# Kernel optimization log

Hardware: AMD Instinct MI355X
Metric: run time of the kernel (lower is better)

## Reference

```python
import jax, jax.numpy as jnp
import numpy as np

NUM_GROUPS = 8
EPS = 1e-5


def setup_inputs() -> dict:
    key = jax.random.key(0)
    ks = jax.random.split(key, 3)
    B, C, H, W = 32, 256, 64, 64
    x = jax.random.normal(ks[0], (B, C, H, W), dtype=jnp.float32)
    gn_weight = jnp.ones((C,), dtype=jnp.float32)
    gn_bias = jnp.zeros((C,), dtype=jnp.float32)
    # 1x1 convs stored as [out_ch, in_ch] matrices (kernel dims squeezed)
    qkv_weight = jax.random.normal(ks[1], (3 * C, C), dtype=jnp.float32) * (1.0 / np.sqrt(C))
    qkv_bias = jnp.zeros((3 * C,), dtype=jnp.float32)
    proj_weight = jax.random.normal(ks[2], (C, C), dtype=jnp.float32) * (1.0 / np.sqrt(C))
    proj_bias = jnp.zeros((C,), dtype=jnp.float32)
    return {
        "x": x,
        "gn_weight": gn_weight,
        "gn_bias": gn_bias,
        "qkv_weight": qkv_weight,
        "qkv_bias": qkv_bias,
        "proj_weight": proj_weight,
        "proj_bias": proj_bias,
    }


def _group_norm(x, weight, bias):
    B, C, H, W = x.shape
    g = x.reshape(B, NUM_GROUPS, C // NUM_GROUPS, H, W)
    mean = g.mean(axis=(2, 3, 4), keepdims=True)
    var = g.var(axis=(2, 3, 4), keepdims=True)
    g = (g - mean) * jax.lax.rsqrt(var + EPS)
    x = g.reshape(B, C, H, W)
    return x * weight[None, :, None, None] + bias[None, :, None, None]


def reference(x, gn_weight, gn_bias, qkv_weight, qkv_bias, proj_weight, proj_bias):
    B, C, H, W = x.shape
    x_norm = _group_norm(x, gn_weight, gn_bias)
    # 1x1 conv C -> 3C: contraction over channel dim
    qkv = jnp.einsum('bchw,oc->bohw', x_norm, qkv_weight) + qkv_bias[None, :, None, None]
    qkv = qkv.reshape(B, 3, C, H * W)  # [B,3,C,HW]
    q, k, v = qkv[:, 0], qkv[:, 1], qkv[:, 2]  # each [B,C,HW]
    # channel attention: attn is [B,C,C], softmax over last (key-channel) dim
    scale = 1.0 / jnp.sqrt(jnp.asarray(C, dtype=x.dtype))
    scores = jnp.einsum('bcn,bdn->bcd', q, k) * scale
    attn = jax.nn.softmax(scores, axis=-1)
    out = jnp.einsum('bcd,bdn->bcn', attn, v).reshape(B, C, H, W)
    proj = jnp.einsum('bchw,oc->bohw', out, proj_weight) + proj_bias[None, :, None, None]
    return x + proj
```

## Files before the change

### kernel.cpp

```cpp
#include <hip/hip_runtime.h>


#define B_ 32
#define C_ 256
#define N_ 4096
#define GSIZE (32 * N_)
#define EPSV 1e-5f
#define SCALE 0.0625f

#define OFF_SC    0
#define OFF_SH    8192
#define OFF_RS    16384
#define OFF_RSP   24576
#define OFF_SQP   90112
#define OFF_RALL  155648
#define OFF_CV    180224
#define OFF_CONST 188416
#define OFF_WVT   196608
#define OFF_GM    229376
#define OFF_AT    2326528
#define OFF_S16   4423680
#define OFF_GP    5472256

typedef _Float16 half_t;
typedef half_t f16x8 __attribute__((ext_vector_type(8)));
typedef float f32x16 __attribute__((ext_vector_type(16)));

__global__ __launch_bounds__(512, 1) void gram_v4_k(const float* __restrict__ x,
                                                    float* __restrict__ ws) {
  __shared__ __align__(16) char hb[2][32768];
  int b = blockIdx.x >> 3, ks = blockIdx.x & 7;
  int t = threadIdx.x;
  const float* xb = x + (size_t)b * (C_ * (size_t)N_) + ks * 512;
  int lane = t & 63, w = t >> 6;
  int wm = w >> 2, wn = w & 3, r31 = lane & 31, hi = lane >> 5;
  int lrow = t >> 4, lc4 = t & 15;
  const float* lbase = xb + (size_t)lrow * N_ + lc4 * 4;
  f32x16 acc[4][2] = {};
  float4 stg[2][8];
  float rs[8] = {0.f, 0.f, 0.f, 0.f, 0.f, 0.f, 0.f, 0.f};
  float rq[8] = {0.f, 0.f, 0.f, 0.f, 0.f, 0.f, 0.f, 0.f};

#define LOADV(sb, c)                                                      \
  _Pragma("unroll") for (int p = 0; p < 8; ++p)                           \
      stg[sb][p] = *(const float4*)(lbase + (size_t)p * 32 * N_ + (c) * 64);

#define WRITEV(sb, buf)                                                   \
  {                                                                       \
    char* bp = hb[buf];                                                   \
    _Pragma("unroll") for (int p = 0; p < 8; ++p) {                       \
      float4 v = stg[sb][p];                                              \
      rs[p] += v.x + v.y + v.z + v.w;                                     \
      rq[p] += v.x * v.x + v.y * v.y + v.z * v.z + v.w * v.w;             \
      union { half_t h[4]; uint2 u; } H;                                  \
      H.h[0] = (half_t)v.x; H.h[1] = (half_t)v.y;                         \
      H.h[2] = (half_t)v.z; H.h[3] = (half_t)v.w;                         \
      int row = lrow + p * 32;                                            \
      int slot = (lc4 >> 1) ^ (row & 7);                                  \
      *(uint2*)(bp + row * 128 + slot * 16 + (lc4 & 1) * 8) = H.u;        \
    }                                                                     \
  }

  LOADV(0, 0);
  LOADV(1, 1);
  WRITEV(0, 0);
  __syncthreads();
  for (int c = 0; c < 8; ++c) {
    int buf = c & 1;
#pragma unroll
    for (int kk = 0; kk < 4; ++kk) {
      int kb = kk * 32 + hi * 16;
      f16x8 Af[4], Bf[2];
#pragma unroll
      for (int m = 0; m < 4; ++m) {
        int row = wm * 128 + m * 32 + r31;
        Af[m] = *(const f16x8*)(hb[buf] + row * 128 + (((kb >> 4) ^ (row & 7)) * 16));
      }
#pragma unroll
      for (int n = 0; n < 2; ++n) {
        int row = wn * 64 + n * 32 + r31;
        Bf[n] = *(const f16x8*)(hb[buf] + row * 128 + (((kb >> 4) ^ (row & 7)) * 16));
      }
#pragma unroll
      for (int m = 0; m < 4; ++m)
#pragma unroll
        for (int n = 0; n < 2; ++n)
          acc[m][n] = __builtin_amdgcn_mfma_f32_32x32x16_f16(Af[m], Bf[n], acc[m][n], 0, 0, 0);
    }
    if (c < 7) {
      int nb = (c + 1) & 1;
      WRITEV(nb, nb);
      if (c < 6) LOADV(buf, c + 2);
      __syncthreads();
    }
  }
#pragma unroll
  for (int p = 0; p < 8; ++p) {
    float s = rs[p], q = rq[p];
    s += __shfl_xor(s, 1); s += __shfl_xor(s, 2);
    s += __shfl_xor(s, 4); s += __shfl_xor(s, 8);
    q += __shfl_xor(q, 1); q += __shfl_xor(q, 2);
    q += __shfl_xor(q, 4); q += __shfl_xor(q, 8);
    if ((t & 15) == 0) {
      int row = lrow + p * 32;
      ws[OFF_RSP + (size_t)blockIdx.x * 256 + row] = s;
      ws[OFF_SQP + (size_t)blockIdx.x * 256 + row] = q;
    }
  }
  half_t* Gp = (half_t*)(ws + OFF_GP) + (size_t)blockIdx.x * 65536;
#pragma unroll
  for (int m = 0; m < 4; ++m)
#pragma unroll
    for (int n = 0; n < 2; ++n)
#pragma unroll
      for (int r = 0; r < 16; ++r) {
        int gr = wm * 128 + m * 32 + (r & 3) + 8 * (r >> 2) + 4 * hi;
        int gc = wn * 64 + n * 32 + r31;
        Gp[gr * 256 + gc] = (half_t)acc[m][n][r];
      }
#undef LOADV
#undef WRITEV
}

__global__ __launch_bounds__(256) void gsum_k(float* __restrict__ ws) {
  int bx = blockIdx.x;
  int b = bx >> 6, seg = bx & 63;
  int e0 = seg * 1024 + threadIdx.x * 4;
  const half_t* Gp = (const half_t*)(ws + OFF_GP) + (size_t)b * 8 * 65536 + e0;
  float4 s = {0.f, 0.f, 0.f, 0.f};
#pragma unroll
  for (int ks = 0; ks < 8; ++ks) {
    union { uint2 u; half_t h[4]; } P;
    P.u = *(const uint2*)(Gp + (size_t)ks * 65536);
    s.x += (float)P.h[0]; s.y += (float)P.h[1];
    s.z += (float)P.h[2]; s.w += (float)P.h[3];
  }
  *(float4*)(ws + OFF_GM + (size_t)b * 65536 + e0) = s;
}

__global__ __launch_bounds__(256) void prep_k(const float* __restrict__ gw,
                                              const float* __restrict__ gb,
                                              const float* __restrict__ qkvw,
                                              float* __restrict__ ws) {
  int b = blockIdx.x, t = threadIdx.x;
  __shared__ float sL[256], qL[256], svecs[256], gmean[8], grstd[8];
  float s = 0.f, q = 0.f;
#pragma unroll
  for (int ks = 0; ks < 8; ++ks) {
    s += ws[OFF_RSP + (b * 8 + ks) * 256 + t];
    q += ws[OFF_SQP + (b * 8 + ks) * 256 + t];
  }
  ws[OFF_RS + b * 256 + t] = s;
  sL[t] = s; qL[t] = q;
  __syncthreads();
  if (t < 8) {
    float gs = 0.f, gq = 0.f;
    for (int i = 0; i < 32; ++i) { gs += sL[t * 32 + i]; gq += qL[t * 32 + i]; }
    float mean = gs * (1.f / GSIZE);
    float var = gq * (1.f / GSIZE) - mean * mean;
    gmean[t] = mean;
    grstd[t] = rsqrtf(var + EPSV);
  }
  __syncthreads();
  int g = t >> 5;
  float sc = grstd[g] * gw[t];
  float sh = gb[t] - gmean[g] * sc;
  ws[OFF_SC + b * 256 + t] = sc;
  ws[OFF_SH + b * 256 + t] = sh;
  float sv = s * sc + 4096.f * sh;
  svecs[t] = sv;
  __syncthreads();
  for (int oo = 0; oo < 3; ++oo) {
    int o = t + oo * 256;
    const float* wr = qkvw + (size_t)o * 256;
    float acc = 0.f;
#pragma unroll 8
    for (int c = 0; c < 256; ++c) acc += wr[c] * svecs[c];
    ws[OFF_RALL + b * 768 + o] = acc;
  }
}

__global__ __launch_bounds__(256) void wvt_k(const float* __restrict__ qkvw,
                                             float* __restrict__ ws) {
  int e = blockIdx.x, d = threadIdx.x;
  float v = qkvw[(size_t)(512 + d) * 256 + e];
  ((half_t*)(ws + OFF_WVT))[e * 256 + d] = (half_t)v;
}

__global__ __launch_bounds__(256) void fused_logits_k(
    const float* __restrict__ qkvw, const float* __restrict__ qkvb,
    float* __restrict__ ws) {
  int b = blockIdx.y, r0 = blockIdx.x * 32;
  int t = threadIdx.x, lane = t & 63, w = t >> 6, r31 = lane & 31, hi = lane >> 5;
  __shared__ __align__(16) char GHL[32768];
  __shared__ __align__(16) char AHL[8192];
  __shared__ float T1s[32][257];
  __shared__ float scs[256], shs[256], rss[256];
  __shared__ float bk_s[256], rk_s[256], bq_s[32], rq_s[32];
  scs[t] = ws[OFF_SC + b * 256 + t];
  shs[t] = ws[OFF_SH + b * 256 + t];
  rss[t] = ws[OFF_RS + b * 256 + t];
  bk_s[t] = qkvb[256 + t];
  rk_s[t] = ws[OFF_RALL + b * 768 + 256 + t];
  if (t < 32) {
    bq_s[t] = qkvb[r0 + t];
    rq_s[t] = ws[OFF_RALL + b * 768 + r0 + t];
  }
  __syncthreads();
  const float* Graw = ws + OFF_GM + (size_t)b * 65536;
  f32x16 acc[2] = {};
  for (int k0 = 0; k0 < 256; k0 += 32) {
    {
      int row = t >> 3, c4 = t & 7;
      float4 v = *(const float4*)(qkvw + (size_t)(r0 + row) * 256 + k0 + c4 * 4);
      union { half_t h[4]; uint2 u; } H, L;
      float vv[4] = {v.x, v.y, v.z, v.w};
#pragma unroll
      for (int j = 0; j < 4; ++j) {
        half_t h = (half_t)vv[j];
        H.h[j] = h; L.h[j] = (half_t)(vv[j] - (float)h);
      }
      int s8 = row & 7;
      *(uint2*)(AHL + row * 128 + (((c4 >> 1) ^ s8) * 16) + (c4 & 1) * 8) = H.u;
      *(uint2*)(AHL + row * 128 + ((((c4 >> 1) + 4) ^ s8) * 16) + (c4 & 1) * 8) = L.u;
    }
    {
#pragma unroll
      for (int p = 0; p < 8; ++p) {
        int f = t + p * 256;
        int row = f >> 3, c4 = f & 7;
        float4 gv = *(const float4*)(Graw + (size_t)row * 256 + k0 + c4 * 4);
        float scd = scs[row], shd = shs[row], rsd = rss[row];
        union { half_t h[4]; uint2 u; } H, L;
        float gvv[4] = {gv.x, gv.y, gv.z, gv.w};
#pragma unroll
        for (int j = 0; j < 4; ++j) {
          int cc = k0 + c4 * 4 + j;
          float scc = scs[cc], shc = shs[cc];
          float val = scc * scd * gvv[j] + scc * shd * rss[cc] +
                      shc * scd * rsd + 4096.f * shc * shd;
          half_t h = (half_t)val;
          H.h[j] = h; L.h[j] = (half_t)(val - (float)h);
        }
        int s8 = row & 7;
        *(uint2*)(GHL + row * 128 + (((c4 >> 1) ^ s8) * 16) + (c4 & 1) * 8) = H.u;
        *(uint2*)(GHL + row * 128 + ((((c4 >> 1) + 4) ^ s8) * 16) + (c4 & 1) * 8) = L.u;
      }
    }
    __syncthreads();
#pragma unroll
    for (int kk = 0; kk < 2; ++kk) {
      int kb = kk * 32 + hi * 16;
      int arow = r31;
      f16x8 Aq = *(const f16x8*)(AHL + arow * 128 + (((kb >> 4) ^ (arow & 7)) * 16));
#pragma unroll
      for (int n = 0; n < 2; ++n) {
        int row = w * 64 + n * 32 + r31;
        int s8 = row & 7;
        f16x8 Bh = *(const f16x8*)(GHL + row * 128 + (((kb >> 4) ^ s8) * 16));
        f16x8 Bl = *(const f16x8*)(GHL + row * 128 + ((((kb >> 4) + 4) ^ s8) * 16));
        acc[n] = __builtin_amdgcn_mfma_f32_32x32x16_f16(Aq, Bh, acc[n], 0, 0, 0);
        acc[n] = __builtin_amdgcn_mfma_f32_32x32x16_f16(Aq, Bl, acc[n], 0, 0, 0);
      }
    }
    __syncthreads();
  }
#pragma unroll
  for (int n = 0; n < 2; ++n)
#pragma unroll
    for (int r = 0; r < 16; ++r)
      T1s[(r & 3) + 8 * (r >> 2) + 4 * hi][w * 64 + n * 32 + r31] = acc[n][r];
  __syncthreads();
  f32x16 acc2[2] = {};
  for (int k0 = 0; k0 < 256; k0 += 64) {
    {
      int row = t >> 3;
#pragma unroll
      for (int u = 0; u < 2; ++u) {
        int c4 = (t & 7) + u * 8;
        float vv[4];
#pragma unroll
        for (int j = 0; j < 4; ++j) vv[j] = T1s[row][k0 + c4 * 4 + j];
        union { half_t h[4]; uint2 u2; } H, L;
#pragma unroll
        for (int j = 0; j < 4; ++j) {
          half_t h = (half_t)vv[j];
          H.h[j] = h; L.h[j] = (half_t)(vv[j] - (float)h);
        }
        int s16 = row & 15;
        *(uint2*)(AHL + row * 256 + (((c4 >> 1) ^ s16) * 16) + (c4 & 1) * 8) = H.u2;
        *(uint2*)(AHL + row * 256 + ((((c4 >> 1) + 8) ^ s16) * 16) + (c4 & 1) * 8) = L.u2;
      }
    }
    {
#pragma unroll
      for (int p = 0; p < 16; ++p) {
        int f = t + p * 256;
        int row = f >> 4, c4 = f & 15;
        float4 v = *(const float4*)(qkvw + (size_t)(256 + row) * 256 + k0 + c4 * 4);
        union { half_t h[4]; uint2 u; } H;
        H.h[0] = (half_t)v.x; H.h[1] = (half_t)v.y;
        H.h[2] = (half_t)v.z; H.h[3] = (half_t)v.w;
        int slot = (c4 >> 1) ^ (row & 7);
        *(uint2*)(GHL + row * 128 + slot * 16 + (c4 & 1) * 8) = H.u;
      }
    }
    __syncthreads();
#pragma unroll
    for (int kk = 0; kk < 4; ++kk) {
      int kb = kk * 32 + hi * 16;
      int arow = r31;
      int s16 = arow & 15;
      f16x8 Ah = *(const f16x8*)(AHL + arow * 256 + (((kb >> 4) ^ s16) * 16));
      f16x8 Al = *(const f16x8*)(AHL + arow * 256 + ((((kb >> 4) + 8) ^ s16) * 16));
#pragma unroll
      for (int n = 0; n < 2; ++n) {
        int row = w * 64 + n * 32 + r31;
        f16x8 Bf = *(const f16x8*)(GHL + row * 128 + (((kb >> 4) ^ (row & 7)) * 16));
        acc2[n] = __builtin_amdgcn_mfma_f32_32x32x16_f16(Ah, Bf, acc2[n], 0, 0, 0);
        acc2[n] = __builtin_amdgcn_mfma_f32_32x32x16_f16(Al, Bf, acc2[n], 0, 0, 0);
      }
    }
    __syncthreads();
  }
#pragma unroll
  for (int n = 0; n < 2; ++n)
#pragma unroll
    for (int r = 0; r < 16; ++r) {
      int rr = (r & 3) + 8 * (r >> 2) + 4 * hi;
      int cc = w * 64 + n * 32 + r31;
      float v = acc2[n][r];
      v = (v + bq_s[rr] * rk_s[cc] + bk_s[cc] * rq_s[rr] +
           4096.f * bq_s[rr] * bk_s[cc]) * SCALE;
      T1s[rr][cc] = v;
    }
  __syncthreads();
  bk_s[t] = qkvb[512 + t];
  __syncthreads();
  {
    int row = t >> 3, ls = t & 7;
    float m = -1e30f;
#pragma unroll
    for (int i = 0; i < 32; ++i) m = fmaxf(m, T1s[row][ls + i * 8]);
    m = fmaxf(m, __shfl_xor(m, 1));
    m = fmaxf(m, __shfl_xor(m, 2));
    m = fmaxf(m, __shfl_xor(m, 4));
    float s = 0.f, cvp = 0.f;
#pragma unroll
    for (int i = 0; i < 32; ++i) {
      int col = ls + i * 8;
      float e = __expf(T1s[row][col] - m);
      T1s[row][col] = e;
      s += e;
      cvp += e * bk_s[col];
    }
    s += __shfl_xor(s, 1); s += __shfl_xor(s, 2); s += __shfl_xor(s, 4);
    cvp += __shfl_xor(cvp, 1); cvp += __shfl_xor(cvp, 2); cvp += __shfl_xor(cvp, 4);
    float inv = 1.f / s;
#pragma unroll
    for (int i = 0; i < 32; ++i) T1s[row][ls + i * 8] *= inv;
    if (ls == 0) ws[OFF_CV + b * 256 + r0 + row] = cvp * inv;
  }
  __syncthreads();
  {
    float* ATb = ws + OFF_AT + (size_t)b * 65536;
#pragma unroll
    for (int u = 0; u < 8; ++u) {
      float4 v = {T1s[u * 4 + 0][t], T1s[u * 4 + 1][t], T1s[u * 4 + 2][t],
                  T1s[u * 4 + 3][t]};
      *(float4*)(ATb + (size_t)t * 256 + r0 + u * 4) = v;
    }
  }
}

__global__ __launch_bounds__(256) void fused_s_k(const float* __restrict__ pw,
                                                 const float* __restrict__ pb,
                                                 float* __restrict__ ws) {
  int b = blockIdx.y, r0 = blockIdx.x * 32;
  int t = threadIdx.x, lane = t & 63, w = t >> 6, r31 = lane & 31, hi = lane >> 5;
  __shared__ __align__(16) char GHL[32768];
  __shared__ __align__(16) char AHL[8192];
  __shared__ float T1s[32][257];
  __shared__ float cvs[256];
  cvs[t] = ws[OFF_CV + b * 256 + t];
  __syncthreads();
  const float* ATb = ws + OFF_AT + (size_t)b * 65536;
  f32x16 acc[2] = {};
  for (int k0 = 0; k0 < 256; k0 += 64) {
    {
#pragma unroll
      for (int p = 0; p < 2; ++p) {
        int f = t + p * 256;
        int row = f >> 4, c4 = f & 15;
        float4 v = *(const float4*)(pw + (size_t)(r0 + row) * 256 + k0 + c4 * 4);
        union { half_t h[4]; uint2 u; } H;
        H.h[0] = (half_t)v.x; H.h[1] = (half_t)v.y;
        H.h[2] = (half_t)v.z; H.h[3] = (half_t)v.w;
        int slot = (c4 >> 1) ^ (row & 7);
        *(uint2*)(AHL + row * 128 + slot * 16 + (c4 & 1) * 8) = H.u;
      }
    }
    {
#pragma unroll
      for (int p = 0; p < 16; ++p) {
        int f = t + p * 256;
        int row = f >> 4, c4 = f & 15;
        float4 v = *(const float4*)(ATb + (size_t)row * 256 + k0 + c4 * 4);
        union { half_t h[4]; uint2 u; } H;
        H.h[0] = (half_t)v.x; H.h[1] = (half_t)v.y;
        H.h[2] = (half_t)v.z; H.h[3] = (half_t)v.w;
        int slot = (c4 >> 1) ^ (row & 7);
        *(uint2*)(GHL + row * 128 + slot * 16 + (c4 & 1) * 8) = H.u;
      }
    }
    __syncthreads();
#pragma unroll
    for (int kk = 0; kk < 4; ++kk) {
      int kb = kk * 32 + hi * 16;
      int arow = r31;
      f16x8 Af = *(const f16x8*)(AHL + arow * 128 + (((kb >> 4) ^ (arow & 7)) * 16));
#pragma unroll
      for (int n = 0; n < 2; ++n) {
        int row = w * 64 + n * 32 + r31;
        f16x8 Bf = *(const f16x8*)(GHL + row * 128 + (((kb >> 4) ^ (row & 7)) * 16));
        acc[n] = __builtin_amdgcn_mfma_f32_32x32x16_f16(Af, Bf, acc[n], 0, 0, 0);
      }
    }
    __syncthreads();
  }
#pragma unroll
  for (int n = 0; n < 2; ++n)
#pragma unroll
    for (int r = 0; r < 16; ++r)
      T1s[(r & 3) + 8 * (r >> 2) + 4 * hi][w * 64 + n * 32 + r31] = acc[n][r];
  __syncthreads();
  {
    int row = t >> 3, ls = t & 7;
    float a = 0.f;
#pragma unroll
    for (int i = 0; i < 32; ++i) {
      int c = ls + i * 8;
      a += pw[(size_t)(r0 + row) * 256 + c] * cvs[c];
    }
    a += __shfl_xor(a, 1); a += __shfl_xor(a, 2); a += __shfl_xor(a, 4);
    if (ls == 0) ws[OFF_CONST + b * 256 + r0 + row] = a + pb[r0 + row];
  }
  const half_t* WVT = (const half_t*)(ws + OFF_WVT);
  f32x16 acc2[2] = {};
  for (int k0 = 0; k0 < 256; k0 += 64) {
    {
      int row = t >> 3;
#pragma unroll
      for (int u = 0; u < 2; ++u) {
        int c4 = (t & 7) + u * 8;
        float vv[4];
#pragma unroll
        for (int j = 0; j < 4; ++j) vv[j] = T1s[row][k0 + c4 * 4 + j];
        union { half_t h[4]; uint2 u2; } H, L;
#pragma unroll
        for (int j = 0; j < 4; ++j) {
          half_t h = (half_t)vv[j];
          H.h[j] = h; L.h[j] = (half_t)(vv[j] - (float)h);
        }
        int s16 = row & 15;
        *(uint2*)(AHL + row * 256 + (((c4 >> 1) ^ s16) * 16) + (c4 & 1) * 8) = H.u2;
        *(uint2*)(AHL + row * 256 + ((((c4 >> 1) + 8) ^ s16) * 16) + (c4 & 1) * 8) = L.u2;
      }
    }
    {
#pragma unroll
      for (int p = 0; p < 8; ++p) {
        int f = t + p * 256;
        int row = f >> 3, h8 = f & 7;
        uint2 v = *(const uint2*)(WVT + (size_t)row * 256 + k0 + h8 * 8);
        uint2 v2 = *(const uint2*)(WVT + (size_t)row * 256 + k0 + h8 * 8 + 4);
        int slot = h8 ^ (row & 7);
        *(uint2*)(GHL + row * 128 + slot * 16) = v;
        *(uint2*)(GHL + row * 128 + slot * 16 + 8) = v2;
      }
    }
    __syncthreads();
#pragma unroll
    for (int kk = 0; kk < 4; ++kk) {
      int kb = kk * 32 + hi * 16;
      int arow = r31;
      int s16 = arow & 15;
      f16x8 Ah = *(const f16x8*)(AHL + arow * 256 + (((kb >> 4) ^ s16) * 16));
      f16x8 Al = *(const f16x8*)(AHL + arow * 256 + ((((kb >> 4) + 8) ^ s16) * 16));
#pragma unroll
      for (int n = 0; n < 2; ++n) {
        int row = w * 64 + n * 32 + r31;
        f16x8 Bf = *(const f16x8*)(GHL + row * 128 + (((kb >> 4) ^ (row & 7)) * 16));
        acc2[n] = __builtin_amdgcn_mfma_f32_32x32x16_f16(Ah, Bf, acc2[n], 0, 0, 0);
        acc2[n] = __builtin_amdgcn_mfma_f32_32x32x16_f16(Al, Bf, acc2[n], 0, 0, 0);
      }
    }
    __syncthreads();
  }
#pragma unroll
  for (int n = 0; n < 2; ++n)
#pragma unroll
    for (int r = 0; r < 16; ++r)
      T1s[(r & 3) + 8 * (r >> 2) + 4 * hi][w * 64 + n * 32 + r31] = acc2[n][r];
  __syncthreads();
  {
    half_t* Sb = (half_t*)(ws + OFF_S16) + (size_t)b * 65536;
    int row = t >> 3, seg = t & 7;
#pragma unroll
    for (int u = 0; u < 4; ++u) {
      union { half_t h[8]; uint4 v; } P;
#pragma unroll
      for (int j = 0; j < 8; ++j)
        P.h[j] = (half_t)T1s[row][seg * 32 + u * 8 + j];
      *(uint4*)(Sb + (size_t)(r0 + row) * 256 + seg * 32 + u * 8) = P.v;
    }
  }
}

__global__ __launch_bounds__(256, 3) void final_mfma_k(
    const float* __restrict__ x, float* __restrict__ out,
    const float* __restrict__ ws) {
  __shared__ __align__(16) char Bt[16384];
  int b = blockIdx.y, n0 = blockIdx.x * 64;
  int t = threadIdx.x, lane = t & 63, w = t >> 6;
  int r31 = lane & 31, hi = lane >> 5;
  const half_t* Shb = (const half_t*)(ws + OFF_S16) + (size_t)b * 65536;
  const float* xb = x + (size_t)b * (C_ * (size_t)N_);
  const float* scb = ws + OFF_SC + b * 256;
  const float* shb = ws + OFF_SH + b * 256;
  f32x16 acc[2][2] = {};
  for (int c0 = 0; c0 < 256; c0 += 128) {
#pragma unroll
    for (int p = 0; p < 8; ++p) {
      int f = t + p * 256;
      int cl = f >> 4, j4 = f & 15;
      int c = c0 + cl;
      float4 v = *(const float4*)(xb + (size_t)c * N_ + n0 + j4 * 4);
      float sc = scb[c], sh = shb[c];
      float vv[4] = {v.x * sc + sh, v.y * sc + sh, v.z * sc + sh, v.w * sc + sh};
      int cb = cl * 2, b16 = cb & ~15, off = cb & 15;
#pragma unroll
      for (int e = 0; e < 4; ++e) {
        int nn = j4 * 4 + e;
        *(half_t*)(Bt + nn * 256 + (b16 ^ ((nn & 15) << 4)) + off) = (half_t)vv[e];
      }
    }
    __syncthreads();
#pragma unroll
    for (int kk = 0; kk < 8; ++kk) {
      int byte = kk * 32 + hi * 16;
      int cA = c0 + kk * 16 + hi * 8;
      f16x8 Af[2], Bf[2];
#pragma unroll
      for (int m = 0; m < 2; ++m) {
        int o = w * 64 + m * 32 + r31;
        Af[m] = *(const f16x8*)(Shb + (size_t)o * 256 + cA);
      }
#pragma unroll
      for (int n = 0; n < 2; ++n) {
        int nn = n * 32 + r31;
        Bf[n] = *(const f16x8*)(Bt + nn * 256 + (byte ^ ((nn & 15) << 4)));
      }
#pragma unroll
      for (int m = 0; m < 2; ++m)
#pragma unroll
        for (int n = 0; n < 2; ++n)
          acc[m][n] = __builtin_amdgcn_mfma_f32_32x32x16_f16(Af[m], Bf[n], acc[m][n], 0, 0, 0);
    }
    __syncthreads();
  }
  float* ob = out + (size_t)b * (C_ * (size_t)N_);
  const float* cstb = ws + OFF_CONST + b * 256;
#pragma unroll
  for (int m = 0; m < 2; ++m)
#pragma unroll
    for (int r = 0; r < 16; ++r) {
      int o = w * 64 + m * 32 + (r & 3) + 8 * (r >> 2) + 4 * hi;
      float cv = cstb[o];
      size_t base = (size_t)o * N_ + n0;
#pragma unroll
      for (int n = 0; n < 2; ++n) {
        int col = n * 32 + r31;
        ob[base + col] = acc[m][n][r] + xb[base + col] + cv;
      }
    }
}

extern "C" void kernel_launch(void* const* d_in, const int* in_sizes, int n_in,
                              void* d_out, int out_size, void* d_ws,
                              size_t ws_size, hipStream_t stream) {
  const float* x = (const float*)d_in[0];
  const float* gw = (const float*)d_in[1];
  const float* gb = (const float*)d_in[2];
  const float* qkvw = (const float*)d_in[3];
  const float* qkvb = (const float*)d_in[4];
  const float* pw = (const float*)d_in[5];
  const float* pb = (const float*)d_in[6];
  float* out = (float*)d_out;
  float* ws = (float*)d_ws;

  hipLaunchKernelGGL(gram_v4_k, dim3(256), dim3(512), 0, stream, x, ws);
  hipLaunchKernelGGL(prep_k, dim3(32), dim3(256), 0, stream, gw, gb, qkvw, ws);
  hipLaunchKernelGGL(gsum_k, dim3(2048), dim3(256), 0, stream, ws);
  hipLaunchKernelGGL(wvt_k, dim3(256), dim3(256), 0, stream, qkvw, ws);
  hipLaunchKernelGGL(fused_logits_k, dim3(8, 32), dim3(256), 0, stream, qkvw, qkvb, ws);
  hipLaunchKernelGGL(fused_s_k, dim3(8, 32), dim3(256), 0, stream, pw, pb, ws);
  hipLaunchKernelGGL(final_mfma_k, dim3(64, 32), dim3(256), 0, stream, x, out, ws);
}
```

Baseline: 252.0 us.

## Fold group-norm affine into S matrix and constant, simplify final GEMM staging

Folds the per-channel group-norm scale into the S matrix columns and the shift into the per-output constant inside fused_s_k. The final kernel can then stage raw x as fp16 without any normalization arithmetic. The final kernel also loads the whole 256-channel tile into shared memory in one pass, using a padded layout instead of the XOR swizzle, and prefetches the next A fragments from global memory. This removes the per-element affine and one barrier pair in the final pass, but uses more LDS, does scalar LDS reads for B fragments, and applies the fp16 rounding to S*scale and raw x instead of to the normalized x.

```diff
diff --git a/kernel.cpp b/kernel.cpp
--- a/kernel.cpp
+++ b/kernel.cpp
@@ -381,8 +381,10 @@
   __shared__ __align__(16) char GHL[32768];
   __shared__ __align__(16) char AHL[8192];
   __shared__ float T1s[32][257];
-  __shared__ float cvs[256];
+  __shared__ float cvs[256], scv[256], shv[256];
   cvs[t] = ws[OFF_CV + b * 256 + t];
+  scv[t] = ws[OFF_SC + b * 256 + t];
+  shv[t] = ws[OFF_SH + b * 256 + t];
   __syncthreads();
   const float* ATb = ws + OFF_AT + (size_t)b * 65536;
   f32x16 acc[2] = {};
@@ -434,6 +436,7 @@
     for (int r = 0; r < 16; ++r)
       T1s[(r & 3) + 8 * (r >> 2) + 4 * hi][w * 64 + n * 32 + r31] = acc[n][r];
   __syncthreads();
+  float cfull = 0.f;
   {
     int row = t >> 3, ls = t & 7;
     float a = 0.f;
@@ -443,7 +446,7 @@
       a += pw[(size_t)(r0 + row) * 256 + c] * cvs[c];
     }
     a += __shfl_xor(a, 1); a += __shfl_xor(a, 2); a += __shfl_xor(a, 4);
-    if (ls == 0) ws[OFF_CONST + b * 256 + r0 + row] = a + pb[r0 + row];
+    cfull = a + pb[r0 + row];
   }
   const half_t* WVT = (const half_t*)(ws + OFF_WVT);
   f32x16 acc2[2] = {};
@@ -506,68 +509,81 @@
   {
     half_t* Sb = (half_t*)(ws + OFF_S16) + (size_t)b * 65536;
     int row = t >> 3, seg = t & 7;
+    float dsh = 0.f;
 #pragma unroll
     for (int u = 0; u < 4; ++u) {
       union { half_t h[8]; uint4 v; } P;
 #pragma unroll
-      for (int j = 0; j < 8; ++j)
-        P.h[j] = (half_t)T1s[row][seg * 32 + u * 8 + j];
+      for (int j = 0; j < 8; ++j) {
+        int col = seg * 32 + u * 8 + j;
+        float sv = T1s[row][col];
+        dsh += sv * shv[col];
+        P.h[j] = (half_t)(sv * scv[col]);
+      }
       *(uint4*)(Sb + (size_t)(r0 + row) * 256 + seg * 32 + u * 8) = P.v;
     }
-  }
-}
-
-__global__ __launch_bounds__(256, 3) void final_mfma_k(
+    dsh += __shfl_xor(dsh, 1); dsh += __shfl_xor(dsh, 2); dsh += __shfl_xor(dsh, 4);
+    if (seg == 0) ws[OFF_CONST + b * 256 + r0 + row] = cfull + dsh;
+  }
+}
+
+__global__ __launch_bounds__(256, 3) void final_v2_k(
     const float* __restrict__ x, float* __restrict__ out,
     const float* __restrict__ ws) {
-  __shared__ __align__(16) char Bt[16384];
+  __shared__ __align__(16) half_t xs[256 * 68];
   int b = blockIdx.y, n0 = blockIdx.x * 64;
   int t = threadIdx.x, lane = t & 63, w = t >> 6;
   int r31 = lane & 31, hi = lane >> 5;
-  const half_t* Shb = (const half_t*)(ws + OFF_S16) + (size_t)b * 65536;
+  const half_t* Sb = (const half_t*)(ws + OFF_S16) + (size_t)b * 65536;
   const float* xb = x + (size_t)b * (C_ * (size_t)N_);
-  const float* scb = ws + OFF_SC + b * 256;
-  const float* shb = ws + OFF_SH + b * 256;
+#pragma unroll
+  for (int h = 0; h < 2; ++h) {
+    float4 v[8];
+#pragma unroll
+    for (int p = 0; p < 8; ++p) {
+      int f = t + (h * 8 + p) * 256;
+      int c = f >> 4, q = f & 15;
+      v[p] = *(const float4*)(xb + (size_t)c * N_ + n0 + q * 4);
+    }
+#pragma unroll
+    for (int p = 0; p < 8; ++p) {
+      int f = t + (h * 8 + p) * 256;
+      int c = f >> 4, q = f & 15;
+      union { half_t hh[4]; uint2 u; } H;
+      H.hh[0] = (half_t)v[p].x; H.hh[1] = (half_t)v[p].y;
+      H.hh[2] = (half_t)v[p].z; H.hh[3] = (half_t)v[p].w;
+      *(uint2*)(&xs[c * 68 + q * 4]) = H.u;
+    }
+  }
+  __syncthreads();
   f32x16 acc[2][2] = {};
-  for (int c0 = 0; c0 < 256; c0 += 128) {
-#pragma unroll
-    for (int p = 0; p < 8; ++p) {
-      int f = t + p * 256;
-      int cl = f >> 4, j4 = f & 15;
-      int c = c0 + cl;
-      float4 v = *(const float4*)(xb + (size_t)c * N_ + n0 + j4 * 4);
-      float sc = scb[c], sh = shb[c];
-      float vv[4] = {v.x * sc + sh, v.y * sc + sh, v.z * sc + sh, v.w * sc + sh};
-      int cb = cl * 2, b16 = cb & ~15, off = cb & 15;
-#pragma unroll
-      for (int e = 0; e < 4; ++e) {
-        int nn = j4 * 4 + e;
-        *(half_t*)(Bt + nn * 256 + (b16 ^ ((nn & 15) << 4)) + off) = (half_t)vv[e];
-      }
-    }
-    __syncthreads();
-#pragma unroll
-    for (int kk = 0; kk < 8; ++kk) {
-      int byte = kk * 32 + hi * 16;
-      int cA = c0 + kk * 16 + hi * 8;
-      f16x8 Af[2], Bf[2];
-#pragma unroll
-      for (int m = 0; m < 2; ++m) {
-        int o = w * 64 + m * 32 + r31;
-        Af[m] = *(const f16x8*)(Shb + (size_t)o * 256 + cA);
-      }
-#pragma unroll
-      for (int n = 0; n < 2; ++n) {
-        int nn = n * 32 + r31;
-        Bf[n] = *(const f16x8*)(Bt + nn * 256 + (byte ^ ((nn & 15) << 4)));
-      }
+  int obase = w * 64;
+  f16x8 An[2];
+#pragma unroll
+  for (int m = 0; m < 2; ++m)
+    An[m] = *(const f16x8*)(Sb + (size_t)(obase + m * 32 + r31) * 256 + hi * 8);
+#pragma unroll 4
+  for (int kk = 0; kk < 16; ++kk) {
+    f16x8 Af[2] = {An[0], An[1]};
+    if (kk < 15) {
+      int cknx = (kk + 1) * 16 + hi * 8;
 #pragma unroll
       for (int m = 0; m < 2; ++m)
-#pragma unroll
-        for (int n = 0; n < 2; ++n)
-          acc[m][n] = __builtin_amdgcn_mfma_f32_32x32x16_f16(Af[m], Bf[n], acc[m][n], 0, 0, 0);
-    }
-    __syncthreads();
+        An[m] = *(const f16x8*)(Sb + (size_t)(obase + m * 32 + r31) * 256 + cknx);
+    }
+    int ck = kk * 16 + hi * 8;
+    f16x8 Bf[2];
+#pragma unroll
+    for (int n = 0; n < 2; ++n) {
+      int col = n * 32 + r31;
+#pragma unroll
+      for (int j = 0; j < 8; ++j) Bf[n][j] = xs[(ck + j) * 68 + col];
+    }
+#pragma unroll
+    for (int m = 0; m < 2; ++m)
+#pragma unroll
+      for (int n = 0; n < 2; ++n)
+        acc[m][n] = __builtin_amdgcn_mfma_f32_32x32x16_f16(Af[m], Bf[n], acc[m][n], 0, 0, 0);
   }
   float* ob = out + (size_t)b * (C_ * (size_t)N_);
   const float* cstb = ws + OFF_CONST + b * 256;
@@ -575,7 +591,7 @@
   for (int m = 0; m < 2; ++m)
 #pragma unroll
     for (int r = 0; r < 16; ++r) {
-      int o = w * 64 + m * 32 + (r & 3) + 8 * (r >> 2) + 4 * hi;
+      int o = obase + m * 32 + (r & 3) + 8 * (r >> 2) + 4 * hi;
       float cv = cstb[o];
       size_t base = (size_t)o * N_ + n0;
 #pragma unroll
@@ -605,5 +621,5 @@
   hipLaunchKernelGGL(wvt_k, dim3(256), dim3(256), 0, stream, qkvw, ws);
   hipLaunchKernelGGL(fused_logits_k, dim3(8, 32), dim3(256), 0, stream, qkvw, qkvb, ws);
   hipLaunchKernelGGL(fused_s_k, dim3(8, 32), dim3(256), 0, stream, pw, pb, ws);
-  hipLaunchKernelGGL(final_mfma_k, dim3(64, 32), dim3(256), 0, stream, x, out, ws);
-}
+  hipLaunchKernelGGL(final_v2_k, dim3(64, 32), dim3(256), 0, stream, x, out, ws);
+}
```

Result: no change. 255.1 us (+1.3%).
